# Kernel optimization log

Hardware: AMD Instinct MI355X
Metric: run time of the kernel (lower is better)

The kernel has to match this reference:

```python
import jax, jax.numpy as jnp
import numpy as np

EMBED_DIM = 1024
NUM_HEADS = 16
HEAD_DIM = EMBED_DIM // NUM_HEADS


def setup_inputs() -> dict:
    key = jax.random.key(0)
    ks = jax.random.split(key, 6)
    B, S, D = 2, 2048, EMBED_DIM
    scale = 1.0 / np.sqrt(D)
    return {
        "inputs": jax.random.normal(ks[0], (B, S, D), dtype=jnp.float32),
        "Wq": jax.random.normal(ks[1], (D, D), dtype=jnp.float32) * scale,
        "Wk": jax.random.normal(ks[2], (D, D), dtype=jnp.float32) * scale,
        "Wv": jax.random.normal(ks[3], (D, D), dtype=jnp.float32) * scale,
        "Wo": jax.random.normal(ks[4], (D, D), dtype=jnp.float32) * scale,
        "bo": jnp.zeros((D,), dtype=jnp.float32),
    }


def reference(inputs, Wq, Wk, Wv, Wo, bo):
    B, S, D = inputs.shape
    H, P = NUM_HEADS, HEAD_DIM
    # torch Linear: x @ W.T ; weights stored [out, in]
    q = inputs @ Wq.T
    k = inputs @ Wk.T
    v = inputs @ Wv.T
    # separate heads: [B, S, H, P] -> [B, H, S, P]
    q = q.reshape(B, S, H, P).transpose(0, 2, 1, 3)
    k = k.reshape(B, S, H, P).transpose(0, 2, 1, 3)
    v = v.reshape(B, S, H, P).transpose(0, 2, 1, 3)
    # scaled dot-product attention; scale = 1/sqrt(P + 1e-9)
    scale = 1.0 / jnp.sqrt(jnp.float32(P) + 1e-9)
    scores = jnp.einsum("bhsp,bhtp->bhst", q, k) * scale
    weights = jax.nn.softmax(scores, axis=-1)
    attn = jnp.einsum("bhst,bhtp->bhsp", weights, v)
    # merge heads -> [B, S, D]
    concat = attn.transpose(0, 2, 1, 3).reshape(B, S, D)
    return concat @ Wo.T + bo
```

## Files before the change

kernel.cpp:

```cpp
#include <hip/hip_runtime.h>
#include <hip/hip_bf16.h>

typedef __bf16 bf16;
typedef __bf16 bf16x4 __attribute__((ext_vector_type(4)));
typedef __bf16 bf16x8 __attribute__((ext_vector_type(8)));
typedef short  s16x4  __attribute__((ext_vector_type(4)));
typedef float  f32x4  __attribute__((ext_vector_type(4)));

#define QSCALE 0.18033688011112042f

__device__ __forceinline__ float exp2_raw(float x) {
    return __builtin_amdgcn_exp2f(x);
}

__device__ __forceinline__ void load16_lds(const bf16* g, bf16* l) {
    __builtin_amdgcn_global_load_lds(
        (const __attribute__((address_space(1))) unsigned int*)g,
        (__attribute__((address_space(3))) unsigned int*)l, 16, 0, 0);
}

__global__ void cvt_f32_bf16(
    const float* __restrict__ s0, const float* __restrict__ s1,
    const float* __restrict__ s2, const float* __restrict__ s3,
    const float* __restrict__ s4,
    bf16* __restrict__ d0, bf16* __restrict__ d1, bf16* __restrict__ d2,
    bf16* __restrict__ d3, bf16* __restrict__ d4)
{
    int blk = blockIdx.x;
    const float* s; bf16* d; int off;
    if (blk < 2048) {
        s = s0; d = d0; off = blk;
    } else {
        int t = (blk - 2048) >> 9;
        off   = (blk - 2048) & 511;
        switch (t) {
            case 0:  s = s1; d = d1; break;
            case 1:  s = s2; d = d2; break;
            case 2:  s = s3; d = d3; break;
            default: s = s4; d = d4; break;
        }
    }
    int idx = off * 256 + threadIdx.x;
    float4 a = ((const float4*)s)[idx * 2];
    float4 b = ((const float4*)s)[idx * 2 + 1];
    bf16x8 o;
    o[0] = (bf16)a.x; o[1] = (bf16)a.y; o[2] = (bf16)a.z; o[3] = (bf16)a.w;
    o[4] = (bf16)b.x; o[5] = (bf16)b.y; o[6] = (bf16)b.z; o[7] = (bf16)b.w;
    *(bf16x8*)&d[idx * 8] = o;
}

__global__ __launch_bounds__(256, 3) void qkv_gemm(
    const bf16* __restrict__ A,
    const bf16* __restrict__ Wq, const bf16* __restrict__ Wk,
    const bf16* __restrict__ Wv,
    bf16* __restrict__ qbuf, bf16* __restrict__ kbuf, bf16* __restrict__ vT)
{
    __shared__ bf16 sA[128 * 32];
    __shared__ bf16 sB[128 * 32];

    const int hwflat = blockIdx.y * 24 + blockIdx.x;
    const int xcd    = hwflat & 7;
    const int slot   = hwflat >> 3;
    const int my     = xcd * 4 + slot / 24;
    const int mx     = slot % 24;

    const int which = mx >> 3;
    const int n0    = (mx & 7) * 128;
    const int m0    = my * 128;
    const bf16* B   = (which == 0) ? Wq : (which == 1) ? Wk : Wv;

    const int tid  = threadIdx.x;
    const int lane = tid & 63;
    const int w    = tid >> 6;
    const int wr   = w >> 1, wc = w & 1;
    const int r    = lane & 15;
    const int qd   = lane >> 4;

    f32x4 acc[4][4];
    const f32x4 zero4 = {0.f, 0.f, 0.f, 0.f};
#pragma unroll
    for (int mi = 0; mi < 4; ++mi)
#pragma unroll
        for (int ni = 0; ni < 4; ++ni) acc[mi][ni] = zero4;

    for (int kt = 0; kt < 32; ++kt) {
        const bf16* gA = A + (size_t)m0 * 1024 + kt * 32;
        const bf16* gB = B + (size_t)n0 * 1024 + kt * 32;
        __syncthreads();
#pragma unroll
        for (int j = 0; j < 2; ++j) {
            int task = j * 256 + tid;
            int row  = task >> 2, ch = task & 3;
            int ldsb = (j * 256 + w * 64) * 8;
            load16_lds(gA + (size_t)row * 1024 + ch * 8, &sA[ldsb]);
            load16_lds(gB + (size_t)row * 1024 + ch * 8, &sB[ldsb]);
        }
        __syncthreads();

        bf16x8 af[4], bfr[4];
#pragma unroll
        for (int mi = 0; mi < 4; ++mi)
            af[mi] = *(const bf16x8*)&sA[(wr * 64 + mi * 16 + r) * 32 + qd * 8];
#pragma unroll
        for (int ni = 0; ni < 4; ++ni)
            bfr[ni] = *(const bf16x8*)&sB[(wc * 64 + ni * 16 + r) * 32 + qd * 8];
#pragma unroll
        for (int mi = 0; mi < 4; ++mi)
#pragma unroll
            for (int ni = 0; ni < 4; ++ni)
                acc[mi][ni] = __builtin_amdgcn_mfma_f32_16x16x32_bf16(
                    af[mi], bfr[ni], acc[mi][ni], 0, 0, 0);
    }

    const float scale = (which == 0) ? QSCALE : 1.0f;
#pragma unroll
    for (int mi = 0; mi < 4; ++mi)
#pragma unroll
        for (int ni = 0; ni < 4; ++ni) {
            int rb  = m0 + wr * 64 + mi * 16 + qd * 4;
            int col = n0 + wc * 64 + ni * 16 + r;
            if (which == 2) {
                bf16x4 pv;
#pragma unroll
                for (int i = 0; i < 4; ++i) pv[i] = (bf16)acc[mi][ni][i];
                *(bf16x4*)&vT[((size_t)((rb >> 11) * 1024 + col)) * 2048 + (rb & 2047)] = pv;
            } else {
                bf16* dst = (which == 0) ? qbuf : kbuf;
#pragma unroll
                for (int i = 0; i < 4; ++i)
                    dst[(size_t)(rb + i) * 1024 + col] = (bf16)(acc[mi][ni][i] * scale);
            }
        }
}

__global__ __launch_bounds__(256, 3) void out_gemm(
    const bf16* __restrict__ A, const bf16* __restrict__ B,
    float* __restrict__ C, const float* __restrict__ bias)
{
    __shared__ bf16 sA[128 * 32];
    __shared__ bf16 sB[64 * 32];

    const int hwflat = blockIdx.y * 16 + blockIdx.x;
    const int xcd    = hwflat & 7;
    const int slot   = hwflat >> 3;
    const int m0     = (xcd * 4 + (slot >> 4)) * 128;
    const int n0     = (slot & 15) * 64;

    const int tid  = threadIdx.x;
    const int lane = tid & 63;
    const int w    = tid >> 6;
    const int wr   = w >> 1, wc = w & 1;
    const int r    = lane & 15;
    const int qd   = lane >> 4;

    f32x4 acc[4][2];
    const f32x4 zero4 = {0.f, 0.f, 0.f, 0.f};
#pragma unroll
    for (int mi = 0; mi < 4; ++mi)
#pragma unroll
        for (int ni = 0; ni < 2; ++ni) acc[mi][ni] = zero4;

    for (int kt = 0; kt < 32; ++kt) {
        const bf16* gA = A + (size_t)m0 * 1024 + kt * 32;
        const bf16* gB = B + (size_t)n0 * 1024 + kt * 32;
        __syncthreads();
#pragma unroll
        for (int j = 0; j < 2; ++j) {
            int task = j * 256 + tid;
            int row  = task >> 2, ch = task & 3;
            int ldsb = (j * 256 + w * 64) * 8;
            load16_lds(gA + (size_t)row * 1024 + ch * 8, &sA[ldsb]);
        }
        {
            int row = tid >> 2, ch = tid & 3;
            int ldsb = (w * 64) * 8;
            load16_lds(gB + (size_t)row * 1024 + ch * 8, &sB[ldsb]);
        }
        __syncthreads();

        bf16x8 af[4], bfr[2];
#pragma unroll
        for (int mi = 0; mi < 4; ++mi)
            af[mi] = *(const bf16x8*)&sA[(wr * 64 + mi * 16 + r) * 32 + qd * 8];
#pragma unroll
        for (int ni = 0; ni < 2; ++ni)
            bfr[ni] = *(const bf16x8*)&sB[(wc * 32 + ni * 16 + r) * 32 + qd * 8];
#pragma unroll
        for (int mi = 0; mi < 4; ++mi)
#pragma unroll
            for (int ni = 0; ni < 2; ++ni)
                acc[mi][ni] = __builtin_amdgcn_mfma_f32_16x16x32_bf16(
                    af[mi], bfr[ni], acc[mi][ni], 0, 0, 0);
    }

#pragma unroll
    for (int mi = 0; mi < 4; ++mi)
#pragma unroll
        for (int ni = 0; ni < 2; ++ni)
#pragma unroll
            for (int i = 0; i < 4; ++i) {
                int row = m0 + wr * 64 + mi * 16 + qd * 4 + i;
                int col = n0 + wc * 32 + ni * 16 + r;
                C[(size_t)row * 1024 + col] = acc[mi][ni][i] + bias[col];
            }
}

__global__ __launch_bounds__(512, 4) void attn_kernel(
    const bf16* __restrict__ qbuf, const bf16* __restrict__ kbuf,
    const bf16* __restrict__ vT, bf16* __restrict__ concat)
{
    __shared__ bf16 sKV[8 * 64 * 72];

    const int tid  = threadIdx.x;
    const int lane = tid & 63;
    const int w    = tid >> 6;
    const int g    = w >> 2;
    const int wq   = w & 3;
    const int gtid = tid & 255;
    const int r    = lane & 15;
    const int qd   = lane >> 4;

    const int hwflat = blockIdx.y * 16 + blockIdx.x;
    const int xcd    = hwflat & 7;
    const int slot   = hwflat >> 3;
    const int bh     = xcd * 4 + (slot >> 4);
    const int qt     = slot & 15;

    const int b    = bh >> 4, h = bh & 15;
    const int qrow0 = b * 2048 + qt * 128;
    const size_t vbase = (size_t)bh * 64 * 2048;

    const s16x4 ones4 = {(short)0x3F80, (short)0x3F80, (short)0x3F80, (short)0x3F80};

    int krow[2], kch[2];
#pragma unroll
    for (int t = 0; t < 2; ++t) {
        int flat = t * 256 + gtid;
        krow[t] = flat >> 3; kch[t] = flat & 7;
    }

    bf16x8 aq[2][2];
#pragma unroll
    for (int mi = 0; mi < 2; ++mi)
#pragma unroll
        for (int ks = 0; ks < 2; ++ks)
            aq[mi][ks] = *(const bf16x8*)&qbuf[
                (size_t)(qrow0 + wq * 32 + mi * 16 + r) * 1024 + h * 64 + ks * 32 + qd * 8];

    f32x4 acc_o[2][4], acc_l[2];
    const f32x4 zero4 = {0.f, 0.f, 0.f, 0.f};
#pragma unroll
    for (int mi = 0; mi < 2; ++mi) {
        acc_l[mi] = zero4;
#pragma unroll
        for (int pj = 0; pj < 4; ++pj) acc_o[mi][pj] = zero4;
    }

    bf16* const myKV = &sKV[g * 4 * 4608];

    bf16x8 rk[2], rv[2];
#pragma unroll
    for (int t = 0; t < 2; ++t) {
        rk[t] = *(const bf16x8*)&kbuf[(size_t)(b * 2048 + g * 64 + krow[t]) * 1024 + h * 64 + kch[t] * 8];
        rv[t] = *(const bf16x8*)&vT[vbase + (size_t)krow[t] * 2048 + g * 64 + kch[t] * 8];
    }
#pragma unroll
    for (int t = 0; t < 2; ++t) {
        *(bf16x8*)&myKV[0 * 4608 + krow[t] * 72 + kch[t] * 8] = rk[t];
        *(bf16x8*)&myKV[1 * 4608 + krow[t] * 72 + kch[t] * 8] = rv[t];
    }
#pragma unroll
    for (int t = 0; t < 2; ++t) {
        rk[t] = *(const bf16x8*)&kbuf[(size_t)(b * 2048 + (2 + g) * 64 + krow[t]) * 1024 + h * 64 + kch[t] * 8];
        rv[t] = *(const bf16x8*)&vT[vbase + (size_t)krow[t] * 2048 + (2 + g) * 64 + kch[t] * 8];
    }
    __syncthreads();

    for (int tt = 0; tt < 16; ++tt) {
        {
            int st = (tt + 1) & 1;
#pragma unroll
            for (int t = 0; t < 2; ++t) {
                *(bf16x8*)&myKV[(2 * st + 0) * 4608 + krow[t] * 72 + kch[t] * 8] = rk[t];
                *(bf16x8*)&myKV[(2 * st + 1) * 4608 + krow[t] * 72 + kch[t] * 8] = rv[t];
            }
        }
        {
            int nxtl = (tt + 2 < 16) ? tt + 2 : 15;
            int gt   = 2 * nxtl + g;
#pragma unroll
            for (int t = 0; t < 2; ++t) {
                rk[t] = *(const bf16x8*)&kbuf[(size_t)(b * 2048 + gt * 64 + krow[t]) * 1024 + h * 64 + kch[t] * 8];
                rv[t] = *(const bf16x8*)&vT[vbase + (size_t)krow[t] * 2048 + gt * 64 + kch[t] * 8];
            }
        }
        const bf16* sK = &myKV[(2 * (tt & 1) + 0) * 4608];
        const bf16* sV = &myKV[(2 * (tt & 1) + 1) * 4608];

        f32x4 accs[2][4];
#pragma unroll
        for (int mi = 0; mi < 2; ++mi)
#pragma unroll
            for (int ni = 0; ni < 4; ++ni) accs[mi][ni] = zero4;
        __builtin_amdgcn_s_setprio(1);
#pragma unroll
        for (int ks = 0; ks < 2; ++ks)
#pragma unroll
            for (int ni = 0; ni < 4; ++ni) {
                bf16x8 ak = *(const bf16x8*)&sK[(ni * 16 + r) * 72 + ks * 32 + qd * 8];
#pragma unroll
                for (int mi = 0; mi < 2; ++mi)
                    accs[mi][ni] = __builtin_amdgcn_mfma_f32_16x16x32_bf16(
                        ak, aq[mi][ks], accs[mi][ni], 0, 0, 0);
            }
        __builtin_amdgcn_s_setprio(0);

        s16x4 pfrag[2][4];
#pragma unroll
        for (int mi = 0; mi < 2; ++mi)
#pragma unroll
            for (int ni = 0; ni < 4; ++ni) {
                bf16x4 pv;
#pragma unroll
                for (int i = 0; i < 4; ++i) pv[i] = (bf16)exp2_raw(accs[mi][ni][i]);
                pfrag[mi][ni] = __builtin_bit_cast(s16x4, pv);
            }

        __builtin_amdgcn_s_setprio(1);
#pragma unroll
        for (int ni = 0; ni < 4; ++ni) {
#pragma unroll
            for (int pj = 0; pj < 4; ++pj) {
                bf16x4 av = *(const bf16x4*)&sV[(pj * 16 + r) * 72 + ni * 16 + qd * 4];
                s16x4  avs = __builtin_bit_cast(s16x4, av);
#pragma unroll
                for (int mi = 0; mi < 2; ++mi)
                    acc_o[mi][pj] = __builtin_amdgcn_mfma_f32_16x16x16bf16_1k(
                        avs, pfrag[mi][ni], acc_o[mi][pj], 0, 0, 0);
            }
#pragma unroll
            for (int mi = 0; mi < 2; ++mi)
                acc_l[mi] = __builtin_amdgcn_mfma_f32_16x16x16bf16_1k(
                    ones4, pfrag[mi][ni], acc_l[mi], 0, 0, 0);
        }
        __builtin_amdgcn_s_setprio(0);

        __syncthreads();
    }

    float* sF = (float*)sKV;
    bf16*  sO = sKV + 18432;

    if (g == 1) {
        int slotc = gtid * 35;
#pragma unroll
        for (int mi = 0; mi < 2; ++mi)
#pragma unroll
            for (int pj = 0; pj < 4; ++pj)
#pragma unroll
                for (int i = 0; i < 4; ++i)
                    sF[slotc + mi * 16 + pj * 4 + i] = acc_o[mi][pj][i];
        sF[slotc + 32] = acc_l[0][0];
        sF[slotc + 33] = acc_l[1][0];
    }
    __syncthreads();
    if (g == 0) {
        int slotc = gtid * 35;
        float inv[2];
#pragma unroll
        for (int mi = 0; mi < 2; ++mi)
            inv[mi] = 1.0f / (acc_l[mi][0] + sF[slotc + 32 + mi]);
#pragma unroll
        for (int mi = 0; mi < 2; ++mi) {
            int qloc = wq * 32 + mi * 16 + r;
#pragma unroll
            for (int pj = 0; pj < 4; ++pj)
#pragma unroll
                for (int i = 0; i < 4; ++i) {
                    float o = acc_o[mi][pj][i] + sF[slotc + mi * 16 + pj * 4 + i];
                    sO[qloc * 72 + pj * 16 + qd * 4 + i] = (bf16)(o * inv[mi]);
                }
        }
    }
    __syncthreads();
    {
        int row = tid >> 2;
        int q4  = tid & 3;
        size_t cb = (size_t)(qrow0 + row) * 1024 + h * 64 + q4 * 16;
        *(bf16x8*)&concat[cb]     = *(const bf16x8*)&sO[row * 72 + q4 * 16];
        *(bf16x8*)&concat[cb + 8] = *(const bf16x8*)&sO[row * 72 + q4 * 16 + 8];
    }
}

extern "C" void kernel_launch(void* const* d_in, const int* in_sizes, int n_in,
                              void* d_out, int out_size, void* d_ws, size_t ws_size,
                              hipStream_t stream)
{
    const float* x  = (const float*)d_in[0];
    const float* Wq = (const float*)d_in[1];
    const float* Wk = (const float*)d_in[2];
    const float* Wv = (const float*)d_in[3];
    const float* Wo = (const float*)d_in[4];
    const float* bo = (const float*)d_in[5];
    float* out = (float*)d_out;

    char* ws = (char*)d_ws;
    bf16* xb     = (bf16*)(ws);
    bf16* Wqb    = (bf16*)(ws + (8u  << 20));
    bf16* Wkb    = (bf16*)(ws + (10u << 20));
    bf16* Wvb    = (bf16*)(ws + (12u << 20));
    bf16* Wob    = (bf16*)(ws + (14u << 20));
    bf16* qbuf   = (bf16*)(ws + (16u << 20));
    bf16* kbuf   = (bf16*)(ws + (24u << 20));
    bf16* vT     = (bf16*)(ws + (32u << 20));
    bf16* concat = (bf16*)(ws + (40u << 20));

    hipLaunchKernelGGL(cvt_f32_bf16, dim3(4096), dim3(256), 0, stream,
                       x, Wq, Wk, Wv, Wo, xb, Wqb, Wkb, Wvb, Wob);
    hipLaunchKernelGGL(qkv_gemm, dim3(24, 32), dim3(256), 0, stream,
                       xb, Wqb, Wkb, Wvb, qbuf, kbuf, vT);
    hipLaunchKernelGGL(attn_kernel, dim3(16, 32), dim3(512), 0, stream,
                       qbuf, kbuf, vT, concat);
    hipLaunchKernelGGL(out_gemm, dim3(16, 32), dim3(256), 0, stream,
                       concat, Wob, out, bo);
}
```

Baseline: 189.2 us.

## Double-buffer LDS tiles in projection GEMMs and stage V transpose through LDS

Both the QKV and output GEMMs now prefetch the next K-slice into a second LDS buffer while the MFMAs run on the current one, which cuts the barriers per iteration from two to one and hides global-load latency. The V-projection epilogue first writes its transposed tile into padded LDS and then stores contiguous 16-byte rows to vT, replacing the scattered 8-byte stores. QKV shared memory becomes dynamic (34816 bytes), and the extra LDS per block may lower occupancy.

Measured after the change: 188.0 us. No clear change (-0.6%).

```diff
diff --git a/kernel.cpp b/kernel.cpp
--- a/kernel.cpp
+++ b/kernel.cpp
@@ -55,8 +55,7 @@
     const bf16* __restrict__ Wv,
     bf16* __restrict__ qbuf, bf16* __restrict__ kbuf, bf16* __restrict__ vT)
 {
-    __shared__ bf16 sA[128 * 32];
-    __shared__ bf16 sB[128 * 32];
+    extern __shared__ bf16 smem[];
 
     const int hwflat = blockIdx.y * 24 + blockIdx.x;
     const int xcd    = hwflat & 7;
@@ -76,6 +75,9 @@
     const int r    = lane & 15;
     const int qd   = lane >> 4;
 
+    const int row0 = tid >> 2,         ch0 = tid & 3;
+    const int row1 = (256 + tid) >> 2, ch1 = tid & 3;
+
     f32x4 acc[4][4];
     const f32x4 zero4 = {0.f, 0.f, 0.f, 0.f};
 #pragma unroll
@@ -83,62 +85,100 @@
 #pragma unroll
         for (int ni = 0; ni < 4; ++ni) acc[mi][ni] = zero4;
 
+    {
+        const bf16* gA = A + (size_t)m0 * 1024;
+        const bf16* gB = B + (size_t)n0 * 1024;
+        load16_lds(gA + (size_t)row0 * 1024 + ch0 * 8, &smem[(0 * 256 + w * 64) * 8]);
+        load16_lds(gA + (size_t)row1 * 1024 + ch1 * 8, &smem[(1 * 256 + w * 64) * 8]);
+        load16_lds(gB + (size_t)row0 * 1024 + ch0 * 8, &smem[8192 + (0 * 256 + w * 64) * 8]);
+        load16_lds(gB + (size_t)row1 * 1024 + ch1 * 8, &smem[8192 + (1 * 256 + w * 64) * 8]);
+    }
+    __syncthreads();
+
     for (int kt = 0; kt < 32; ++kt) {
-        const bf16* gA = A + (size_t)m0 * 1024 + kt * 32;
-        const bf16* gB = B + (size_t)n0 * 1024 + kt * 32;
-        __syncthreads();
-#pragma unroll
-        for (int j = 0; j < 2; ++j) {
-            int task = j * 256 + tid;
-            int row  = task >> 2, ch = task & 3;
-            int ldsb = (j * 256 + w * 64) * 8;
-            load16_lds(gA + (size_t)row * 1024 + ch * 8, &sA[ldsb]);
-            load16_lds(gB + (size_t)row * 1024 + ch * 8, &sB[ldsb]);
-        }
-        __syncthreads();
-
+        if (kt < 31) {
+            int st = (kt + 1) & 1;
+            const bf16* gA = A + (size_t)m0 * 1024 + (kt + 1) * 32;
+            const bf16* gB = B + (size_t)n0 * 1024 + (kt + 1) * 32;
+            bf16* dA = &smem[st * 4096];
+            bf16* dB = &smem[8192 + st * 4096];
+            load16_lds(gA + (size_t)row0 * 1024 + ch0 * 8, &dA[(0 * 256 + w * 64) * 8]);
+            load16_lds(gA + (size_t)row1 * 1024 + ch1 * 8, &dA[(1 * 256 + w * 64) * 8]);
+            load16_lds(gB + (size_t)row0 * 1024 + ch0 * 8, &dB[(0 * 256 + w * 64) * 8]);
+            load16_lds(gB + (size_t)row1 * 1024 + ch1 * 8, &dB[(1 * 256 + w * 64) * 8]);
+        }
+
+        const bf16* cA = &smem[(kt & 1) * 4096];
+        const bf16* cB = &smem[8192 + (kt & 1) * 4096];
         bf16x8 af[4], bfr[4];
 #pragma unroll
         for (int mi = 0; mi < 4; ++mi)
-            af[mi] = *(const bf16x8*)&sA[(wr * 64 + mi * 16 + r) * 32 + qd * 8];
+            af[mi] = *(const bf16x8*)&cA[(wr * 64 + mi * 16 + r) * 32 + qd * 8];
 #pragma unroll
         for (int ni = 0; ni < 4; ++ni)
-            bfr[ni] = *(const bf16x8*)&sB[(wc * 64 + ni * 16 + r) * 32 + qd * 8];
+            bfr[ni] = *(const bf16x8*)&cB[(wc * 64 + ni * 16 + r) * 32 + qd * 8];
 #pragma unroll
         for (int mi = 0; mi < 4; ++mi)
 #pragma unroll
             for (int ni = 0; ni < 4; ++ni)
                 acc[mi][ni] = __builtin_amdgcn_mfma_f32_16x16x32_bf16(
                     af[mi], bfr[ni], acc[mi][ni], 0, 0, 0);
-    }
-
-    const float scale = (which == 0) ? QSCALE : 1.0f;
-#pragma unroll
-    for (int mi = 0; mi < 4; ++mi)
-#pragma unroll
-        for (int ni = 0; ni < 4; ++ni) {
-            int rb  = m0 + wr * 64 + mi * 16 + qd * 4;
-            int col = n0 + wc * 64 + ni * 16 + r;
-            if (which == 2) {
+
+        __syncthreads();
+    }
+
+    if (which == 2) {
+        bf16* sT = smem;
+#pragma unroll
+        for (int mi = 0; mi < 4; ++mi)
+#pragma unroll
+            for (int ni = 0; ni < 4; ++ni) {
+                int colL = wc * 64 + ni * 16 + r;
+                int sL   = wr * 64 + mi * 16 + qd * 4;
                 bf16x4 pv;
 #pragma unroll
                 for (int i = 0; i < 4; ++i) pv[i] = (bf16)acc[mi][ni][i];
-                *(bf16x4*)&vT[((size_t)((rb >> 11) * 1024 + col)) * 2048 + (rb & 2047)] = pv;
-            } else {
-                bf16* dst = (which == 0) ? qbuf : kbuf;
+                *(bf16x4*)&sT[colL * 136 + sL] = pv;
+            }
+        __syncthreads();
+        const int b0 = m0 >> 11, s0 = m0 & 2047;
+#pragma unroll
+        for (int rr = 0; rr < 2; ++rr) {
+            int colL = rr * 64 + (tid >> 2);
+            int q    = tid & 3;
+            bf16* dst = &vT[((size_t)(b0 * 1024 + n0 + colL)) * 2048 + s0];
+            const bf16* src = &sT[colL * 136];
+            bf16x8 v = *(const bf16x8*)&src[q * 8];
+            *(bf16x8*)&dst[q * 8] = v;
+            v = *(const bf16x8*)&src[32 + q * 8];
+            *(bf16x8*)&dst[32 + q * 8] = v;
+            v = *(const bf16x8*)&src[64 + q * 8];
+            *(bf16x8*)&dst[64 + q * 8] = v;
+            v = *(const bf16x8*)&src[96 + q * 8];
+            *(bf16x8*)&dst[96 + q * 8] = v;
+        }
+    } else {
+        const float scale = (which == 0) ? QSCALE : 1.0f;
+        bf16* dst = (which == 0) ? qbuf : kbuf;
+#pragma unroll
+        for (int mi = 0; mi < 4; ++mi)
+#pragma unroll
+            for (int ni = 0; ni < 4; ++ni) {
+                int rb  = m0 + wr * 64 + mi * 16 + qd * 4;
+                int col = n0 + wc * 64 + ni * 16 + r;
 #pragma unroll
                 for (int i = 0; i < 4; ++i)
                     dst[(size_t)(rb + i) * 1024 + col] = (bf16)(acc[mi][ni][i] * scale);
             }
-        }
+    }
 }
 
 __global__ __launch_bounds__(256, 3) void out_gemm(
     const bf16* __restrict__ A, const bf16* __restrict__ B,
     float* __restrict__ C, const float* __restrict__ bias)
 {
-    __shared__ bf16 sA[128 * 32];
-    __shared__ bf16 sB[64 * 32];
+    __shared__ bf16 sA[2][128 * 32];
+    __shared__ bf16 sB[2][64 * 32];
 
     const int hwflat = blockIdx.y * 16 + blockIdx.x;
     const int xcd    = hwflat & 7;
@@ -153,6 +193,9 @@
     const int r    = lane & 15;
     const int qd   = lane >> 4;
 
+    const int row0 = tid >> 2,         ch0 = tid & 3;
+    const int row1 = (256 + tid) >> 2, ch1 = tid & 3;
+
     f32x4 acc[4][2];
     const f32x4 zero4 = {0.f, 0.f, 0.f, 0.f};
 #pragma unroll
@@ -160,37 +203,42 @@
 #pragma unroll
         for (int ni = 0; ni < 2; ++ni) acc[mi][ni] = zero4;
 
+    {
+        const bf16* gA = A + (size_t)m0 * 1024;
+        const bf16* gB = B + (size_t)n0 * 1024;
+        load16_lds(gA + (size_t)row0 * 1024 + ch0 * 8, &sA[0][(0 * 256 + w * 64) * 8]);
+        load16_lds(gA + (size_t)row1 * 1024 + ch1 * 8, &sA[0][(1 * 256 + w * 64) * 8]);
+        load16_lds(gB + (size_t)row0 * 1024 + ch0 * 8, &sB[0][(w * 64) * 8]);
+    }
+    __syncthreads();
+
     for (int kt = 0; kt < 32; ++kt) {
-        const bf16* gA = A + (size_t)m0 * 1024 + kt * 32;
-        const bf16* gB = B + (size_t)n0 * 1024 + kt * 32;
-        __syncthreads();
-#pragma unroll
-        for (int j = 0; j < 2; ++j) {
-            int task = j * 256 + tid;
-            int row  = task >> 2, ch = task & 3;
-            int ldsb = (j * 256 + w * 64) * 8;
-            load16_lds(gA + (size_t)row * 1024 + ch * 8, &sA[ldsb]);
-        }
-        {
-            int row = tid >> 2, ch = tid & 3;
-            int ldsb = (w * 64) * 8;
-            load16_lds(gB + (size_t)row * 1024 + ch * 8, &sB[ldsb]);
-        }
-        __syncthreads();
-
+        if (kt < 31) {
+            int st = (kt + 1) & 1;
+            const bf16* gA = A + (size_t)m0 * 1024 + (kt + 1) * 32;
+            const bf16* gB = B + (size_t)n0 * 1024 + (kt + 1) * 32;
+            load16_lds(gA + (size_t)row0 * 1024 + ch0 * 8, &sA[st][(0 * 256 + w * 64) * 8]);
+            load16_lds(gA + (size_t)row1 * 1024 + ch1 * 8, &sA[st][(1 * 256 + w * 64) * 8]);
+            load16_lds(gB + (size_t)row0 * 1024 + ch0 * 8, &sB[st][(w * 64) * 8]);
+        }
+
+        const bf16* cA = sA[kt & 1];
+        const bf16* cB = sB[kt & 1];
         bf16x8 af[4], bfr[2];
 #pragma unroll
         for (int mi = 0; mi < 4; ++mi)
-            af[mi] = *(const bf16x8*)&sA[(wr * 64 + mi * 16 + r) * 32 + qd * 8];
+            af[mi] = *(const bf16x8*)&cA[(wr * 64 + mi * 16 + r) * 32 + qd * 8];
 #pragma unroll
         for (int ni = 0; ni < 2; ++ni)
-            bfr[ni] = *(const bf16x8*)&sB[(wc * 32 + ni * 16 + r) * 32 + qd * 8];
+            bfr[ni] = *(const bf16x8*)&cB[(wc * 32 + ni * 16 + r) * 32 + qd * 8];
 #pragma unroll
         for (int mi = 0; mi < 4; ++mi)
 #pragma unroll
             for (int ni = 0; ni < 2; ++ni)
                 acc[mi][ni] = __builtin_amdgcn_mfma_f32_16x16x32_bf16(
                     af[mi], bfr[ni], acc[mi][ni], 0, 0, 0);
+
+        __syncthreads();
     }
 
 #pragma unroll
@@ -417,7 +465,7 @@
 
     hipLaunchKernelGGL(cvt_f32_bf16, dim3(4096), dim3(256), 0, stream,
                        x, Wq, Wk, Wv, Wo, xb, Wqb, Wkb, Wvb, Wob);
-    hipLaunchKernelGGL(qkv_gemm, dim3(24, 32), dim3(256), 0, stream,
+    hipLaunchKernelGGL(qkv_gemm, dim3(24, 32), dim3(256), 34816, stream,
                        xb, Wqb, Wkb, Wvb, qbuf, kbuf, vT);
     hipLaunchKernelGGL(attn_kernel, dim3(16, 32), dim3(512), 0, stream,
                        qbuf, kbuf, vT, concat);
```
